# Optimization experiments

Hardware: AMD Instinct MI355X
Metric: run time of the kernel (lower is better)

Reference implementation:

```python
import jax, jax.numpy as jnp
import numpy as np

NUM_USERS = 100000
NUM_ITEMS = 100000
D = 64          # embed_dim
B = 4096        # batch of users (rows of sparse interaction matrix)
NNZ = 204800    # nonzeros in sparse user-item matrix (~50 items/user)
N = 1048576     # number of (user,item) pairs to score
DROPOUT = 0.2


def setup_inputs() -> dict:
    key = jax.random.key(0)
    ks = jax.random.split(key, 10)
    return {
        "user_ids": jax.random.randint(ks[0], (B,), 0, NUM_USERS, dtype=jnp.int32),
        "bat_idx": jax.random.randint(ks[1], (N,), 0, B, dtype=jnp.int32),
        "sp_row": jax.random.randint(ks[2], (NNZ,), 0, B, dtype=jnp.int32),
        "sp_col": jax.random.randint(ks[3], (NNZ,), 0, NUM_ITEMS, dtype=jnp.int32),
        "bat_items": jax.random.randint(ks[4], (N,), 0, NUM_ITEMS, dtype=jnp.int32),
        # learned parameters (normal init for embeddings, zeros for offset/bias, as in reset_parameters)
        "en_emb": jax.random.normal(ks[5], (NUM_ITEMS, D), dtype=jnp.float32) * 0.01,
        "en_offset": jnp.zeros((D,), dtype=jnp.float32),
        "de_emb": jax.random.normal(ks[6], (NUM_ITEMS, D), dtype=jnp.float32) * 0.01,
        "de_bias": jnp.zeros((NUM_ITEMS,), dtype=jnp.float32),
        "user_emb": jax.random.normal(ks[7], (NUM_USERS, D), dtype=jnp.float32) * 0.01,
    }


def reference(user_ids, bat_idx, sp_row, sp_col, bat_items,
              en_emb, en_offset, de_emb, de_bias, user_emb):
    keep = 1.0 - DROPOUT
    # dropout_sparse: bernoulli keep-mask on sparse nnz values (binary 1.0), rescaled by 1/keep
    drop_mask = jax.random.bernoulli(jax.random.key(42), keep, (NNZ,))
    vals = drop_mask.astype(en_emb.dtype) / keep  # corrupted sparse values [NNZ]

    # sparse @ dense: sum_j A[b,j] * en_emb[j]  ->  gather + segment_sum  -> [B, D]
    hidden = jax.ops.segment_sum(vals[:, None] * en_emb[sp_col], sp_row, num_segments=B)
    hidden = jnp.tanh(hidden + user_emb[user_ids] + en_offset[None, :])

    # decode: inner product of gathered hidden rows and item embeddings
    h = hidden[bat_idx]                      # [N, D]
    de_i = de_emb[bat_items]                 # [N, D]
    ratings = jnp.sum(h * de_i, axis=-1) + de_bias[bat_items]  # [N]

    # l2 reg over unique bat_items rows (mask-based == torch.unique gather)
    item_mask = jnp.zeros((NUM_ITEMS,), en_emb.dtype).at[bat_items].set(1.0)
    reg_loss = 0.5 * (
        jnp.sum(item_mask * jnp.sum(en_emb ** 2, axis=-1))
        + jnp.sum(en_offset ** 2)
        + jnp.sum(user_emb[user_ids] ** 2)
        + jnp.sum(item_mask * jnp.sum(de_emb ** 2, axis=-1))
        + jnp.sum(item_mask * de_bias ** 2)
    )
    return ratings, reg_loss
```

## Files before the change

kernel.cpp:

```cpp
#include <hip/hip_runtime.h>
#include <hip/hip_bf16.h>

#define PARTITIONABLE 1
#define NB 8
#define CAPB 136192
#define FATB 2048
#define CAPR 128
#define RSB 200
#define HBLK 1024
#define REGB 256

__device__ __forceinline__ unsigned rotl32(unsigned x, int r) {
    return (x << r) | (x >> (32 - r));
}

__device__ __forceinline__ void threefry2x32(unsigned k0, unsigned k1,
                                             unsigned& x0, unsigned& x1) {
    unsigned ks0 = k0, ks1 = k1, ks2 = k0 ^ k1 ^ 0x1BD11BDAu;
    x0 += ks0; x1 += ks1;
#define TF_R(r) { x0 += x1; x1 = rotl32(x1, r); x1 ^= x0; }
    TF_R(13) TF_R(15) TF_R(26) TF_R(6)   x0 += ks1; x1 += ks2 + 1u;
    TF_R(17) TF_R(29) TF_R(16) TF_R(24)  x0 += ks2; x1 += ks0 + 2u;
    TF_R(13) TF_R(15) TF_R(26) TF_R(6)   x0 += ks0; x1 += ks1 + 3u;
    TF_R(17) TF_R(29) TF_R(16) TF_R(24)  x0 += ks1; x1 += ks2 + 4u;
    TF_R(13) TF_R(15) TF_R(26) TF_R(6)   x0 += ks2; x1 += ks0 + 5u;
#undef TF_R
}

__device__ __forceinline__ bool keep_mask(int i, int nnz) {
#if PARTITIONABLE
    unsigned x0 = 0u, x1 = (unsigned)i;
    threefry2x32(0u, 42u, x0, x1);
    unsigned bits = x0 ^ x1;
#else
    int half = nnz >> 1;
    int j = (i < half) ? i : i - half;
    unsigned x0 = (unsigned)j, x1 = (unsigned)(j + half);
    threefry2x32(0u, 42u, x0, x1);
    unsigned bits = (i < half) ? x0 : x1;
#endif
    float u = __uint_as_float((bits >> 9) | 0x3f800000u) - 1.0f;
    return u < 0.8f;
}

__device__ __forceinline__ unsigned short f2bf(float f) {
    unsigned u = __float_as_uint(f);
    return (unsigned short)((u + 0x7FFFu + ((u >> 16) & 1u)) >> 16);
}

__device__ __forceinline__ float bfdot8(uint4 h, uint4 d) {
    float s;
    s  = __uint_as_float(h.x << 16)         * __uint_as_float(d.x << 16);
    s += __uint_as_float(h.x & 0xFFFF0000u) * __uint_as_float(d.x & 0xFFFF0000u);
    s += __uint_as_float(h.y << 16)         * __uint_as_float(d.y << 16);
    s += __uint_as_float(h.y & 0xFFFF0000u) * __uint_as_float(d.y & 0xFFFF0000u);
    s += __uint_as_float(h.z << 16)         * __uint_as_float(d.z << 16);
    s += __uint_as_float(h.z & 0xFFFF0000u) * __uint_as_float(d.z & 0xFFFF0000u);
    s += __uint_as_float(h.w << 16)         * __uint_as_float(d.w << 16);
    s += __uint_as_float(h.w & 0xFFFF0000u) * __uint_as_float(d.w & 0xFFFF0000u);
    return s;
}

__global__ void k_prep(const int* __restrict__ bat_idx, const int* __restrict__ bat_items,
                       unsigned char* __restrict__ mask, int* __restrict__ cursor,
                       unsigned* __restrict__ perm, unsigned* __restrict__ inv,
                       const int* __restrict__ sp_row, const int* __restrict__ sp_col,
                       int* __restrict__ rowcur, unsigned* __restrict__ srow,
                       int N, int num_items, int nnz, int B) {
    __shared__ int sh[4096];
    if (blockIdx.x < 256) {
        if (threadIdx.x < NB) sh[threadIdx.x] = 0;
        __syncthreads();
        const int per = N / 256;
        const int base_n = blockIdx.x * per;
        const int iters = per / blockDim.x;
        unsigned packed[16];
        int bkt[16];
        for (int it = 0; it < iters; ++it) {
            int n = base_n + it * blockDim.x + threadIdx.x;
            int item = bat_items[n];
            int bidx = bat_idx[n];
            mask[item] = 1;
            int b = (int)(((unsigned long long)(unsigned)item * NB) / (unsigned)num_items);
            packed[it] = ((unsigned)item << 12) | (unsigned)bidx;
            bkt[it] = b;
            atomicAdd(&sh[b], 1);
        }
        __syncthreads();
        if (threadIdx.x < NB) {
            int c = sh[threadIdx.x];
            sh[threadIdx.x] = atomicAdd(&cursor[threadIdx.x], c);
        }
        __syncthreads();
        for (int it = 0; it < iters; ++it) {
            int n = base_n + it * blockDim.x + threadIdx.x;
            int pos = atomicAdd(&sh[bkt[it]], 1);
            unsigned gpos = (unsigned)bkt[it] * CAPB + (unsigned)min(pos, CAPB - 1);
            perm[gpos] = packed[it];
            inv[n] = gpos;
        }
    } else {
        const int blk = blockIdx.x - 256;
        for (int i = threadIdx.x; i < B; i += blockDim.x) sh[i] = 0;
        __syncthreads();
        const int per = nnz / RSB;
        const int base = blk * per;
        const int iters = per / blockDim.x;
        unsigned pk[8];
        int rw[8];
        for (int it = 0; it < iters; ++it) {
            int i = base + it * blockDim.x + threadIdx.x;
            int row = sp_row[i];
            int col = sp_col[i];
            unsigned k = keep_mask(i, nnz) ? 1u : 0u;
            pk[it] = ((unsigned)col << 1) | k;
            rw[it] = row;
            atomicAdd(&sh[row], 1);
        }
        __syncthreads();
        for (int i = threadIdx.x; i < B; i += blockDim.x) {
            int c = sh[i];
            if (c) sh[i] = atomicAdd(&rowcur[i], c);
        }
        __syncthreads();
        for (int it = 0; it < iters; ++it) {
            int pos = atomicAdd(&sh[rw[it]], 1);
            srow[(size_t)rw[it] * CAPR + min(pos, CAPR - 1)] = pk[it];
        }
    }
}

__global__ void k_hidden_reg(const unsigned* __restrict__ srow, const int* __restrict__ rowcur,
                             const float* __restrict__ en_emb, const float* __restrict__ user_emb,
                             const int* __restrict__ user_ids, const float* __restrict__ en_off,
                             unsigned short* __restrict__ hb,
                             const unsigned char* __restrict__ mask,
                             const float* __restrict__ de_emb, const float* __restrict__ de_bias,
                             unsigned short* __restrict__ debf,
                             float* __restrict__ reg_ws, int B, int num_items) {
    if (blockIdx.x < HBLK) {
        const int lane = threadIdx.x & 63;
        const int row = (blockIdx.x * blockDim.x + threadIdx.x) >> 6;
        if (row >= B) return;
        const int cnt = min(rowcur[row], CAPR);
        const unsigned* sr = srow + (size_t)row * CAPR;
        float acc0 = 0.f, acc1 = 0.f, acc2 = 0.f, acc3 = 0.f;
        for (int j0 = 0; j0 < cnt; j0 += 64) {
            unsigned ev = (j0 + lane < cnt) ? sr[j0 + lane] : 0u;
            int m = min(64, cnt - j0);
            int jj = 0;
            for (; jj + 3 < m; jj += 4) {
                unsigned e0 = __shfl(ev, jj);
                unsigned e1 = __shfl(ev, jj + 1);
                unsigned e2 = __shfl(ev, jj + 2);
                unsigned e3 = __shfl(ev, jj + 3);
                if (e0 & 1u) acc0 += en_emb[(size_t)(e0 >> 1) * 64 + lane];
                if (e1 & 1u) acc1 += en_emb[(size_t)(e1 >> 1) * 64 + lane];
                if (e2 & 1u) acc2 += en_emb[(size_t)(e2 >> 1) * 64 + lane];
                if (e3 & 1u) acc3 += en_emb[(size_t)(e3 >> 1) * 64 + lane];
            }
            for (; jj < m; ++jj) {
                unsigned e0 = __shfl(ev, jj);
                if (e0 & 1u) acc0 += en_emb[(size_t)(e0 >> 1) * 64 + lane];
            }
        }
        int uid = user_ids[row];
        float hval = 1.25f * ((acc0 + acc1) + (acc2 + acc3))
                   + user_emb[(size_t)uid * 64 + lane] + en_off[lane];
        hb[(size_t)row * 64 + lane] = f2bf(tanhf(hval));
    } else {
        const int bx = blockIdx.x - HBLK;
        const int stride = REGB * blockDim.x;
        float s = 0.f;
        for (int t = bx * blockDim.x + threadIdx.x; t < num_items * 16; t += stride) {
            int i = t >> 4, l = t & 15;
            float4 d = *reinterpret_cast<const float4*>(de_emb + (size_t)i * 64 + l * 4);
            ushort4 o;
            o.x = f2bf(d.x); o.y = f2bf(d.y); o.z = f2bf(d.z); o.w = f2bf(d.w);
            reinterpret_cast<ushort4*>(debf)[t] = o;
            if (mask[i]) {
                float4 e = *reinterpret_cast<const float4*>(en_emb + (size_t)i * 64 + l * 4);
                s += e.x*e.x + e.y*e.y + e.z*e.z + e.w*e.w
                   + d.x*d.x + d.y*d.y + d.z*d.z + d.w*d.w;
                if (l == 0) { float bb = de_bias[i]; s += bb * bb; }
            }
        }
        for (int t = bx * blockDim.x + threadIdx.x; t < B * 16; t += stride) {
            int b = t >> 4, l = t & 15;
            int uid = user_ids[b];
            float4 u = *reinterpret_cast<const float4*>(user_emb + (size_t)uid * 64 + l * 4);
            s += u.x*u.x + u.y*u.y + u.z*u.z + u.w*u.w;
        }
        if (bx == 0 && threadIdx.x < 64) {
            float o = en_off[threadIdx.x];
            s += o * o;
        }
        for (int m = 1; m < 64; m <<= 1) s += __shfl_xor(s, m);
        __shared__ float wsum[4];
        if ((threadIdx.x & 63) == 0) wsum[threadIdx.x >> 6] = s;
        __syncthreads();
        if (threadIdx.x == 0)
            atomicAdd(reg_ws, wsum[0] + wsum[1] + wsum[2] + wsum[3]);
    }
}

__global__ void k_ratings_bkt(const unsigned short* __restrict__ hb,
                              const unsigned short* __restrict__ debf,
                              const float* __restrict__ de_bias,
                              const unsigned* __restrict__ perm, const int* __restrict__ cursor,
                              float* __restrict__ r_perm) {
    const int bkt = blockIdx.x & (NB - 1);
    const int cnt = cursor[bkt];
    const int l = threadIdx.x & 7;
    const int gid = (blockIdx.x >> 3) * (blockDim.x >> 3) + (threadIdx.x >> 3);
    const int gpb = (gridDim.x >> 3) * (blockDim.x >> 3);
    const unsigned* pb = perm + (size_t)bkt * CAPB;
    float* rb = r_perm + (size_t)bkt * CAPB;

    int slot = gid;
    for (; slot + 3 * gpb < cnt; slot += 4 * gpb) {
        unsigned p0 = pb[slot];
        unsigned p1 = pb[slot + gpb];
        unsigned p2 = pb[slot + 2 * gpb];
        unsigned p3 = pb[slot + 3 * gpb];
        int it0 = (int)(p0 >> 12), b0 = (int)(p0 & 0xFFFu);
        int it1 = (int)(p1 >> 12), b1 = (int)(p1 & 0xFFFu);
        int it2 = (int)(p2 >> 12), b2 = (int)(p2 & 0xFFFu);
        int it3 = (int)(p3 >> 12), b3 = (int)(p3 & 0xFFFu);
        uint4 h0 = *reinterpret_cast<const uint4*>(hb   + (size_t)b0  * 64 + l * 8);
        uint4 d0 = *reinterpret_cast<const uint4*>(debf + (size_t)it0 * 64 + l * 8);
        uint4 h1 = *reinterpret_cast<const uint4*>(hb   + (size_t)b1  * 64 + l * 8);
        uint4 d1 = *reinterpret_cast<const uint4*>(debf + (size_t)it1 * 64 + l * 8);
        uint4 h2 = *reinterpret_cast<const uint4*>(hb   + (size_t)b2  * 64 + l * 8);
        uint4 d2 = *reinterpret_cast<const uint4*>(debf + (size_t)it2 * 64 + l * 8);
        uint4 h3 = *reinterpret_cast<const uint4*>(hb   + (size_t)b3  * 64 + l * 8);
        uint4 d3 = *reinterpret_cast<const uint4*>(debf + (size_t)it3 * 64 + l * 8);
        float s0 = bfdot8(h0, d0);
        float s1 = bfdot8(h1, d1);
        float s2 = bfdot8(h2, d2);
        float s3 = bfdot8(h3, d3);
        s0 += __shfl_xor(s0, 1); s1 += __shfl_xor(s1, 1);
        s2 += __shfl_xor(s2, 1); s3 += __shfl_xor(s3, 1);
        s0 += __shfl_xor(s0, 2); s1 += __shfl_xor(s1, 2);
        s2 += __shfl_xor(s2, 2); s3 += __shfl_xor(s3, 2);
        s0 += __shfl_xor(s0, 4); s1 += __shfl_xor(s1, 4);
        s2 += __shfl_xor(s2, 4); s3 += __shfl_xor(s3, 4);
        if (l == 0) {
            rb[slot]           = s0 + de_bias[it0];
            rb[slot + gpb]     = s1 + de_bias[it1];
            rb[slot + 2 * gpb] = s2 + de_bias[it2];
            rb[slot + 3 * gpb] = s3 + de_bias[it3];
        }
    }
    for (; slot < cnt; slot += gpb) {
        unsigned p = pb[slot];
        int item = (int)(p >> 12), bidx = (int)(p & 0xFFFu);
        uint4 hv = *reinterpret_cast<const uint4*>(hb   + (size_t)bidx * 64 + l * 8);
        uint4 dv = *reinterpret_cast<const uint4*>(debf + (size_t)item * 64 + l * 8);
        float s = bfdot8(hv, dv);
        s += __shfl_xor(s, 1);
        s += __shfl_xor(s, 2);
        s += __shfl_xor(s, 4);
        if (l == 0) rb[slot] = s + de_bias[item];
    }
}

__global__ void k_unperm(const unsigned* __restrict__ inv, const float* __restrict__ r_perm,
                         const float* __restrict__ reg_ws, float* __restrict__ out, int N) {
    const int quads = N >> 2;
    const int stride = gridDim.x * blockDim.x;
    for (int q = blockIdx.x * blockDim.x + threadIdx.x; q < quads; q += stride) {
        uint4 iv = reinterpret_cast<const uint4*>(inv)[q];
        float4 o;
        o.x = r_perm[iv.x];
        o.y = r_perm[iv.y];
        o.z = r_perm[iv.z];
        o.w = r_perm[iv.w];
        reinterpret_cast<float4*>(out)[q] = o;
    }
    if (blockIdx.x == 0 && threadIdx.x == 0)
        out[N] = 0.5f * reg_ws[0];
}

__global__ void k_mask(const int* __restrict__ bat_items, unsigned char* __restrict__ mask,
                       int N) {
    int t = blockIdx.x * blockDim.x + threadIdx.x;
    if (t < N) mask[bat_items[t]] = 1;
}

__global__ void k_ratings(const float* __restrict__ hidden, const float* __restrict__ de_emb,
                          const float* __restrict__ de_bias,
                          const int* __restrict__ bat_idx, const int* __restrict__ bat_items,
                          float* __restrict__ out, int N) {
    const int l = threadIdx.x & 15;
    const int gid = (blockIdx.x * blockDim.x + threadIdx.x) >> 4;
    const int gstride = (gridDim.x * blockDim.x) >> 4;
    for (int n = gid; n < N; n += gstride) {
        int b  = bat_idx[n];
        int it = bat_items[n];
        float4 hv = *reinterpret_cast<const float4*>(hidden + (size_t)b  * 64 + l * 4);
        float4 dv = *reinterpret_cast<const float4*>(de_emb + (size_t)it * 64 + l * 4);
        float s = hv.x*dv.x + hv.y*dv.y + hv.z*dv.z + hv.w*dv.w;
        s += __shfl_xor(s, 1);
        s += __shfl_xor(s, 2);
        s += __shfl_xor(s, 4);
        s += __shfl_xor(s, 8);
        if (l == 0) out[n] = s + de_bias[it];
    }
}

__global__ void k_scatter(const int* __restrict__ sp_row, const int* __restrict__ sp_col,
                          const float* __restrict__ en_emb, float* __restrict__ hidden,
                          int nnz) {
    const int lane = threadIdx.x & 63;
    const int wave = (blockIdx.x * blockDim.x + threadIdx.x) >> 6;
    const int nwaves = (gridDim.x * blockDim.x) >> 6;
    for (int i = wave; i < nnz; i += nwaves) {
        if (!keep_mask(i, nnz)) continue;
        int row = sp_row[i];
        int col = sp_col[i];
        float v = 1.25f * en_emb[(size_t)col * 64 + lane];
        atomicAdd(&hidden[row * 64 + lane], v);
    }
}

__global__ void k_hfinish(float* __restrict__ hidden, const float* __restrict__ user_emb,
                          const int* __restrict__ user_ids, const float* __restrict__ en_off,
                          int B) {
    int t = blockIdx.x * blockDim.x + threadIdx.x;
    if (t >= B * 64) return;
    int b = t >> 6, d = t & 63;
    int uid = user_ids[b];
    float h = hidden[t] + user_emb[(size_t)uid * 64 + d] + en_off[d];
    hidden[t] = tanhf(h);
}

__global__ void k_reg_fb(const unsigned char* __restrict__ mask,
                         const float* __restrict__ en_emb, const float* __restrict__ de_emb,
                         const float* __restrict__ de_bias,
                         const float* __restrict__ user_emb, const int* __restrict__ user_ids,
                         const float* __restrict__ en_off,
                         float* __restrict__ reg, int num_items, int B) {
    const int stride = gridDim.x * blockDim.x;
    float s = 0.f;
    for (int t = blockIdx.x * blockDim.x + threadIdx.x; t < num_items * 16; t += stride) {
        int i = t >> 4, l = t & 15;
        if (mask[i]) {
            float4 e = *reinterpret_cast<const float4*>(en_emb + (size_t)i * 64 + l * 4);
            float4 d = *reinterpret_cast<const float4*>(de_emb + (size_t)i * 64 + l * 4);
            s += e.x*e.x + e.y*e.y + e.z*e.z + e.w*e.w
               + d.x*d.x + d.y*d.y + d.z*d.z + d.w*d.w;
            if (l == 0) { float bb = de_bias[i]; s += bb * bb; }
        }
    }
    for (int t = blockIdx.x * blockDim.x + threadIdx.x; t < B * 16; t += stride) {
        int b = t >> 4, l = t & 15;
        int uid = user_ids[b];
        float4 u = *reinterpret_cast<const float4*>(user_emb + (size_t)uid * 64 + l * 4);
        s += u.x*u.x + u.y*u.y + u.z*u.z + u.w*u.w;
    }
    if (blockIdx.x == 0 && threadIdx.x < 64) {
        float o = en_off[threadIdx.x];
        s += o * o;
    }
    for (int m = 1; m < 64; m <<= 1) s += __shfl_xor(s, m);
    __shared__ float wsum[4];
    if ((threadIdx.x & 63) == 0) wsum[threadIdx.x >> 6] = s;
    __syncthreads();
    if (threadIdx.x == 0)
        atomicAdd(reg, 0.5f * (wsum[0] + wsum[1] + wsum[2] + wsum[3]));
}

extern "C" void kernel_launch(void* const* d_in, const int* in_sizes, int n_in,
                              void* d_out, int out_size, void* d_ws, size_t ws_size,
                              hipStream_t stream) {
    const int*   user_ids  = (const int*)  d_in[0];
    const int*   bat_idx   = (const int*)  d_in[1];
    const int*   sp_row    = (const int*)  d_in[2];
    const int*   sp_col    = (const int*)  d_in[3];
    const int*   bat_items = (const int*)  d_in[4];
    const float* en_emb    = (const float*)d_in[5];
    const float* en_off    = (const float*)d_in[6];
    const float* de_emb    = (const float*)d_in[7];
    const float* de_bias   = (const float*)d_in[8];
    const float* user_emb  = (const float*)d_in[9];

    const int B         = in_sizes[0];
    const int N         = in_sizes[1];
    const int NNZ       = in_sizes[2];
    const int NUM_ITEMS = in_sizes[8];

    float* out = (float*)d_out;

    char* ws = (char*)d_ws;
    size_t off = 0;
    unsigned char* mask = (unsigned char*)(ws + off);
    off += ((size_t)NUM_ITEMS + 255) & ~(size_t)255;
    int* cursor = (int*)(ws + off);               off += 256;
    int* rowcur = (int*)(ws + off);               off += (size_t)B * 4;
    float* reg_ws = (float*)(ws + off);           off += 256;
    const size_t zero_bytes = off;
    float* hidden = (float*)(ws + off);           off += (size_t)B * 64 * 4;
    unsigned* perm   = (unsigned*)(ws + off);     off += (size_t)NB * CAPB * 4;
    unsigned* inv    = (unsigned*)(ws + off);     off += (size_t)N * 4;
    float*    r_perm = (float*)(ws + off);
    unsigned* srow   = (unsigned*)r_perm;
    size_t tail = (size_t)NB * CAPB * 4;
    if ((size_t)B * CAPR * 4 > tail) tail = (size_t)B * CAPR * 4;
    off += tail;
    unsigned short* hb   = (unsigned short*)(ws + off);  off += (size_t)B * 64 * 2;
    off = (off + 15) & ~(size_t)15;
    unsigned short* debf = (unsigned short*)(ws + off);  off += (size_t)NUM_ITEMS * 64 * 2;

    const bool sorted_path =
        (ws_size >= off) && (N == (1 << 20)) && (B == 4096) &&
        (NUM_ITEMS <= (1 << 17)) && (NUM_ITEMS >= 65536) &&
        (NUM_ITEMS % 4 == 0) &&
        (NNZ % (RSB * 256) == 0) && (NNZ / RSB <= CAPR * 256);

    hipMemsetAsync(ws, 0, zero_bytes, stream);

    if (sorted_path) {
        k_prep<<<256 + RSB, 256, 0, stream>>>(
            bat_idx, bat_items, mask, cursor, perm, inv,
            sp_row, sp_col, rowcur, srow, N, NUM_ITEMS, NNZ, B);
        k_hidden_reg<<<HBLK + REGB, 256, 0, stream>>>(
            srow, rowcur, en_emb, user_emb, user_ids, en_off, hb,
            mask, de_emb, de_bias, debf, reg_ws, B, NUM_ITEMS);
        k_ratings_bkt<<<FATB, 256, 0, stream>>>(hb, debf, de_bias, perm, cursor, r_perm);
        k_unperm<<<1024, 256, 0, stream>>>(inv, r_perm, reg_ws, out, N);
    } else {
        hipMemsetAsync(hidden, 0, (size_t)B * 64 * 4, stream);
        hipMemsetAsync(out + N, 0, sizeof(float), stream);
        k_mask<<<(N + 255) / 256, 256, 0, stream>>>(bat_items, mask, N);
        k_scatter<<<FATB, 256, 0, stream>>>(sp_row, sp_col, en_emb, hidden, NNZ);
        k_hfinish<<<(B * 64 + 255) / 256, 256, 0, stream>>>(hidden, user_emb, user_ids,
                                                            en_off, B);
        k_ratings<<<FATB, 256, 0, stream>>>(hidden, de_emb, de_bias, bat_idx, bat_items, out, N);
        k_reg_fb<<<REGB, 256, 0, stream>>>(mask, en_emb, de_emb, de_bias,
                                           user_emb, user_ids, en_off, out + N, NUM_ITEMS, B);
    }
}
```

Before: 193.2 us.

## Drop dropped nnz at bucketing, unroll gather by 8, branchless reg pass

Dropout is now applied when rows are bucketed. Dropped nonzeros are never written to the per-row lists, so the hidden-state gather loops over kept entries only, with no per-entry branch, and is unrolled to 8 independent accumulators. The regularisation pass loads en_emb unconditionally and multiplies by the mask instead of branching, and gets four times as many blocks. The cost is extra en_emb traffic in the reg pass in exchange for less divergence and more parallelism.

```diff
diff --git a/kernel.cpp b/kernel.cpp
--- a/kernel.cpp
+++ b/kernel.cpp
@@ -8,7 +8,7 @@
 #define CAPR 128
 #define RSB 200
 #define HBLK 1024
-#define REGB 256
+#define REGB 1024
 
 __device__ __forceinline__ unsigned rotl32(unsigned x, int r) {
     return (x << r) | (x >> (32 - r));
@@ -112,10 +112,10 @@
             int i = base + it * blockDim.x + threadIdx.x;
             int row = sp_row[i];
             int col = sp_col[i];
-            unsigned k = keep_mask(i, nnz) ? 1u : 0u;
-            pk[it] = ((unsigned)col << 1) | k;
-            rw[it] = row;
-            atomicAdd(&sh[row], 1);
+            bool k = keep_mask(i, nnz);
+            pk[it] = (unsigned)col;
+            rw[it] = k ? row : -1;
+            if (k) atomicAdd(&sh[row], 1);
         }
         __syncthreads();
         for (int i = threadIdx.x; i < B; i += blockDim.x) {
@@ -124,8 +124,10 @@
         }
         __syncthreads();
         for (int it = 0; it < iters; ++it) {
-            int pos = atomicAdd(&sh[rw[it]], 1);
-            srow[(size_t)rw[it] * CAPR + min(pos, CAPR - 1)] = pk[it];
+            if (rw[it] >= 0) {
+                int pos = atomicAdd(&sh[rw[it]], 1);
+                srow[(size_t)rw[it] * CAPR + min(pos, CAPR - 1)] = pk[it];
+            }
         }
     }
 }
@@ -145,27 +147,47 @@
         const int cnt = min(rowcur[row], CAPR);
         const unsigned* sr = srow + (size_t)row * CAPR;
         float acc0 = 0.f, acc1 = 0.f, acc2 = 0.f, acc3 = 0.f;
+        float acc4 = 0.f, acc5 = 0.f, acc6 = 0.f, acc7 = 0.f;
         for (int j0 = 0; j0 < cnt; j0 += 64) {
             unsigned ev = (j0 + lane < cnt) ? sr[j0 + lane] : 0u;
             int m = min(64, cnt - j0);
             int jj = 0;
+            for (; jj + 7 < m; jj += 8) {
+                unsigned e0 = __shfl(ev, jj);
+                unsigned e1 = __shfl(ev, jj + 1);
+                unsigned e2 = __shfl(ev, jj + 2);
+                unsigned e3 = __shfl(ev, jj + 3);
+                unsigned e4 = __shfl(ev, jj + 4);
+                unsigned e5 = __shfl(ev, jj + 5);
+                unsigned e6 = __shfl(ev, jj + 6);
+                unsigned e7 = __shfl(ev, jj + 7);
+                acc0 += en_emb[(size_t)e0 * 64 + lane];
+                acc1 += en_emb[(size_t)e1 * 64 + lane];
+                acc2 += en_emb[(size_t)e2 * 64 + lane];
+                acc3 += en_emb[(size_t)e3 * 64 + lane];
+                acc4 += en_emb[(size_t)e4 * 64 + lane];
+                acc5 += en_emb[(size_t)e5 * 64 + lane];
+                acc6 += en_emb[(size_t)e6 * 64 + lane];
+                acc7 += en_emb[(size_t)e7 * 64 + lane];
+            }
             for (; jj + 3 < m; jj += 4) {
                 unsigned e0 = __shfl(ev, jj);
                 unsigned e1 = __shfl(ev, jj + 1);
                 unsigned e2 = __shfl(ev, jj + 2);
                 unsigned e3 = __shfl(ev, jj + 3);
-                if (e0 & 1u) acc0 += en_emb[(size_t)(e0 >> 1) * 64 + lane];
-                if (e1 & 1u) acc1 += en_emb[(size_t)(e1 >> 1) * 64 + lane];
-                if (e2 & 1u) acc2 += en_emb[(size_t)(e2 >> 1) * 64 + lane];
-                if (e3 & 1u) acc3 += en_emb[(size_t)(e3 >> 1) * 64 + lane];
+                acc0 += en_emb[(size_t)e0 * 64 + lane];
+                acc1 += en_emb[(size_t)e1 * 64 + lane];
+                acc2 += en_emb[(size_t)e2 * 64 + lane];
+                acc3 += en_emb[(size_t)e3 * 64 + lane];
             }
             for (; jj < m; ++jj) {
                 unsigned e0 = __shfl(ev, jj);
-                if (e0 & 1u) acc0 += en_emb[(size_t)(e0 >> 1) * 64 + lane];
+                acc0 += en_emb[(size_t)e0 * 64 + lane];
             }
         }
         int uid = user_ids[row];
-        float hval = 1.25f * ((acc0 + acc1) + (acc2 + acc3))
+        float hval = 1.25f * (((acc0 + acc1) + (acc2 + acc3))
+                            + ((acc4 + acc5) + (acc6 + acc7)))
                    + user_emb[(size_t)uid * 64 + lane] + en_off[lane];
         hb[(size_t)row * 64 + lane] = f2bf(tanhf(hval));
     } else {
@@ -175,15 +197,15 @@
         for (int t = bx * blockDim.x + threadIdx.x; t < num_items * 16; t += stride) {
             int i = t >> 4, l = t & 15;
             float4 d = *reinterpret_cast<const float4*>(de_emb + (size_t)i * 64 + l * 4);
+            float4 e = *reinterpret_cast<const float4*>(en_emb + (size_t)i * 64 + l * 4);
+            float m = (float)mask[i];
             ushort4 o;
             o.x = f2bf(d.x); o.y = f2bf(d.y); o.z = f2bf(d.z); o.w = f2bf(d.w);
             reinterpret_cast<ushort4*>(debf)[t] = o;
-            if (mask[i]) {
-                float4 e = *reinterpret_cast<const float4*>(en_emb + (size_t)i * 64 + l * 4);
-                s += e.x*e.x + e.y*e.y + e.z*e.z + e.w*e.w
-                   + d.x*d.x + d.y*d.y + d.z*d.z + d.w*d.w;
-                if (l == 0) { float bb = de_bias[i]; s += bb * bb; }
-            }
+            float q = e.x*e.x + e.y*e.y + e.z*e.z + e.w*e.w
+                    + d.x*d.x + d.y*d.y + d.z*d.z + d.w*d.w;
+            if (l == 0) { float bb = de_bias[i]; q += bb * bb; }
+            s += m * q;
         }
         for (int t = bx * blockDim.x + threadIdx.x; t < B * 16; t += stride) {
             int b = t >> 4, l = t & 15;
```

Result: faster. 180.6 us (-6.5%).
